# Kernel optimization log

Hardware: AMD Instinct MI355X
Metric: run time of the kernel (lower is better)

## Reference

```python
import jax, jax.numpy as jnp
import numpy as np

B, N, D = 256, 128, 128            # batch, tree nodes (incl. zero-pad node 0), input_feature_dim
MAX_PRED, MAX_COL, MAX_OP = 30, 200, 20
OTHER = D - 2 * MAX_PRED - 1 - 32  # 35
C_IN = D + 64 - 2 * MAX_PRED - 1   # 131 = tree-conv input channels


def setup_inputs() -> dict:
    key = jax.random.key(0)
    ks = jax.random.split(key, 14)
    others = jax.random.normal(ks[0], (B, N, OTHER), dtype=jnp.float32)
    cols = jax.random.randint(ks[1], (B, N, MAX_PRED), 0, MAX_COL).astype(jnp.float32)
    ops = jax.random.randint(ks[2], (B, N, MAX_PRED), 0, MAX_OP).astype(jnp.float32)
    length = jax.random.randint(ks[3], (B, N, 1), 0, MAX_PRED + 1).astype(jnp.float32)
    param = jax.random.normal(ks[4], (B, N, 32), dtype=jnp.float32)
    feature = jnp.concatenate([others, cols, ops, length, param], axis=-1).transpose(0, 2, 1)  # (B, D, N)
    indexes = jax.random.randint(ks[5], (B, 3 * (N - 1), 1), 0, N, dtype=jnp.int32).astype(jnp.int64)

    def conv_w(k, o, i):
        return jax.random.normal(k, (o, i, 3), dtype=jnp.float32) * (1.0 / np.sqrt(3 * i))

    def lin_w(k, o, i):
        return jax.random.normal(k, (o, i), dtype=jnp.float32) * (1.0 / np.sqrt(i))

    return dict(
        feature=feature, indexes=indexes,
        col_embed=jax.random.normal(ks[6], (MAX_COL, 32), dtype=jnp.float32),
        op_embed=jax.random.normal(ks[7], (MAX_OP, 32), dtype=jnp.float32),
        w1=conv_w(ks[8], 256, C_IN), b1=jnp.zeros((256,), jnp.float32),
        w2=conv_w(ks[9], 128, 256), b2=jnp.zeros((128,), jnp.float32),
        w3=conv_w(ks[10], 64, 128), b3=jnp.zeros((64,), jnp.float32),
        fw1=lin_w(ks[11], 32, 64), fb1=jnp.zeros((32,), jnp.float32),
        fw2=lin_w(ks[12], 1, 32), fb2=jnp.zeros((1,), jnp.float32),
    )


def tree_conv(x, idx, w, b):
    # x: (B, C, N); idx: (B, 3M, 1) with M = N-1; w: (O, C, 3)
    Bb, C, _ = x.shape
    g = jnp.take_along_axis(x, idx[:, :, 0][:, None, :], axis=2)        # (B, C, 3M) gather (self,left,right)
    g = g.reshape(Bb, C, -1, 3)                                          # (B, C, M, 3)
    out = jnp.einsum('bcmk,ock->bom', g, w) + b[None, :, None]           # stride-3 kernel-3 conv
    zero = jnp.zeros((Bb, w.shape[0], 1), out.dtype)                     # re-prepend zero-pad node
    return jnp.concatenate([zero, out], axis=2)                          # (B, O, N)


def tree_norm(x):
    # per-sample layernorm over (channel, node) dims, unbiased std (torch.std default)
    mean = jnp.mean(x, axis=(1, 2), keepdims=True)
    std = jnp.std(x, axis=(1, 2), ddof=1, keepdims=True)
    return (x - mean) / (std + 1e-5)


def reference(feature, indexes, col_embed, op_embed, w1, b1, w2, b2, w3, b3, fw1, fb1, fw2, fb2):
    Bb, d, n = feature.shape
    f = feature.transpose(0, 2, 1).reshape(Bb * n, d)
    others = f[:, :OTHER]
    cols = jax.lax.stop_gradient(f[:, OTHER:OTHER + MAX_PRED]).astype(jnp.int32)
    ops = jax.lax.stop_gradient(f[:, OTHER + MAX_PRED:OTHER + 2 * MAX_PRED]).astype(jnp.int32)
    length = f[:, OTHER + 2 * MAX_PRED:OTHER + 2 * MAX_PRED + 1]          # (BN, 1)
    param = f[:, -32:]
    emb = jnp.concatenate([col_embed[cols], op_embed[ops]], axis=-1)      # (BN, P, 64)
    mask = jnp.arange(MAX_PRED)[None, :] < length                         # (BN, P)
    total = jnp.sum(emb * mask[..., None], axis=1)                        # (BN, 64) masked sum
    collate = jnp.concatenate([others, total, param], axis=-1).reshape(Bb, n, -1).transpose(0, 2, 1)  # (B, C_IN, N)

    x = jax.nn.leaky_relu(tree_norm(tree_conv(collate, indexes, w1, b1)), 0.01)
    x = jax.nn.leaky_relu(tree_norm(tree_conv(x, indexes, w2, b2)), 0.01)
    x = tree_norm(tree_conv(x, indexes, w3, b3))                          # (B, 64, N)
    pooled = jnp.max(x, axis=2)                                           # DynamicPooling -> (B, 64)
    h = jax.nn.relu(pooled @ fw1.T + fb1)
    return h @ fw2.T + fb2                                                # (B, 1)
```

## Files before the change

kernel.cpp:

```cpp
#include <hip/hip_runtime.h>
#include <hip/hip_bf16.h>
#include <math.h>

#define B_    256
#define N_    128
#define MAXP  30
#define OTHER_ 35
#define CIN1  131
#define NIDX  381

#define KPAD1 160
#define KPAD2 256
#define KPAD3 128
#define S_IDX (B_ * NIDX)
#define S_P1  (15 * 4 * 4 * 512)
#define S_P2  (24 * 4 * 2 * 512)
#define S_P3  (12 * 4 * 1 * 512)
#define PREP_TOTAL (S_IDX + S_P1 + S_P2 + S_P3)
#define PREP_BLOCKS ((PREP_TOTAL + 511) / 512)
#define EMBED_BLOCKS (B_ * 4)

typedef short short8 __attribute__((ext_vector_type(8)));
typedef float f32x4 __attribute__((ext_vector_type(4)));

__device__ inline void split1(float v, short& h, short& l) {
  unsigned u = __float_as_uint(v);
  unsigned hb = (u + 0x7fffu + ((u >> 16) & 1u)) >> 16;
  float fh = __uint_as_float(hb << 16);
  float r = v - fh;
  unsigned u2 = __float_as_uint(r);
  unsigned lb = (u2 + 0x7fffu + ((u2 >> 16) & 1u)) >> 16;
  h = (short)hb;
  l = (short)lb;
}

__device__ inline void split2(float v, short& h, short& l) {
  __hip_bfloat16 hb = __float2bfloat16(v);
  float fh = __bfloat162float(hb);
  __hip_bfloat16 lb = __float2bfloat16(v - fh);
  __builtin_memcpy(&h, &hb, 2);
  __builtin_memcpy(&l, &lb, 2);
}

template <int KREAL, int KPAD, int SUB, int NWO>
__device__ inline void packw(int l, const float* __restrict__ w,
                             short* __restrict__ oh, short* __restrict__ ol) {
  const int e = l & 7;
  const int lane = (l >> 3) & 63;
  const int x = l >> 9;
  const int su = x % SUB;
  const int y = x / SUB;
  const int g = y % NWO;
  const int gks = y / NWO;
  const int oc = (g * SUB + su) * 16 + (lane & 15);
  const int ctot = gks * 32 + ((lane >> 4) & 3) * 8 + e;
  const int kk = ctot / KPAD;
  const int ch = ctot - kk * KPAD;
  const float v = (ch < KREAL) ? w[(oc * KREAL + ch) * 3 + kk] : 0.f;
  short h, lo;
  split1(v, h, lo);
  oh[l] = h;
  ol[l] = lo;
}

__global__ __launch_bounds__(512) void prep_embed_kernel(
    const float* __restrict__ feature,
    const float* __restrict__ col_embed,
    const float* __restrict__ op_embed,
    short* __restrict__ collateH, short* __restrict__ collateL,
    const void* __restrict__ rawIdx, int* __restrict__ idx32,
    const float* __restrict__ w1, short* __restrict__ w1h, short* __restrict__ w1l,
    const float* __restrict__ w2, short* __restrict__ w2h, short* __restrict__ w2l,
    const float* __restrict__ w3, short* __restrict__ w3h, short* __restrict__ w3l) {
  const int bx = blockIdx.x;
  const int tid = threadIdx.x;

  if (bx >= EMBED_BLOCKS) {
    const int gid = (bx - EMBED_BLOCKS) * 512 + tid;
    if (gid < S_IDX) {
      const int* r32 = (const int*)rawIdx;
      const int lane = tid & 63;
      const int lo = r32[2 * lane];
      const int hi = r32[2 * lane + 1];
      const bool ok = (hi == 0 && lo >= 0 && lo < N_);
      const bool is64 = __all(ok);
      idx32[gid] = is64 ? (int)((const long long*)rawIdx)[gid] : ((const int*)rawIdx)[gid];
    } else if (gid < S_IDX + S_P1) {
      packw<131, KPAD1, 4, 4>(gid - S_IDX, w1, w1h, w1l);
    } else if (gid < S_IDX + S_P1 + S_P2) {
      packw<256, KPAD2, 2, 4>(gid - (S_IDX + S_P1), w2, w2h, w2l);
    } else if (gid < PREP_TOTAL) {
      packw<128, KPAD3, 1, 4>(gid - (S_IDX + S_P1 + S_P2), w3, w3h, w3l);
    }
    return;
  }

  __shared__ float feat[128 * 33];
  __shared__ float ce[200 * 32];
  __shared__ float oe[20 * 32];
  const int b = bx >> 2;
  const int n0 = (bx & 3) * 32;
  const float* fb = feature + (size_t)b * 16384;

  {
    const float4* s = (const float4*)col_embed;
    float4* d = (float4*)ce;
#pragma unroll
    for (int it = 0; it < 4; ++it) {
      const int t = it * 512 + tid;
      if (t < 1600) d[t] = s[t];
    }
    if (tid < 160) ((float4*)oe)[tid] = ((const float4*)op_embed)[tid];
  }
  {
    const int d = tid >> 2;
    const int c8 = (tid & 3) * 8;
    const float4 v0 = *reinterpret_cast<const float4*>(&fb[d * 128 + n0 + c8]);
    const float4 v1 = *reinterpret_cast<const float4*>(&fb[d * 128 + n0 + c8 + 4]);
    float* p = &feat[d * 33 + c8];
    p[0] = v0.x; p[1] = v0.y; p[2] = v0.z; p[3] = v0.w;
    p[4] = v1.x; p[5] = v1.y; p[6] = v1.z; p[7] = v1.w;
  }
  __syncthreads();

  const int wv = tid >> 6;
  const int lane = tid & 63;
  const int cl = lane & 31;

#pragma unroll
  for (int ni = 0; ni < 4; ++ni) {
    const int nl = wv * 4 + ni;
    const int n = n0 + nl;
    int civ = 0, oiv = 0;
    if (lane < MAXP) civ = (int)feat[(OTHER_ + lane) * 33 + nl];
    if (lane >= 32 && lane < 32 + MAXP) oiv = (int)feat[(OTHER_ + MAXP + (lane - 32)) * 33 + nl];
    const int L = (int)feat[95 * 33 + nl];

    float acc = 0.f;
    for (int i = 0; i < L; ++i) {
      const int cv = __shfl(civ, i);
      const int ov = __shfl(oiv, 32 + i);
      acc += (lane < 32) ? ce[cv * 32 + cl] : oe[ov * 32 + cl];
    }

    short* outH = collateH + ((size_t)b * 128 + n) * KPAD1;
    short* outL = collateL + ((size_t)b * 128 + n) * KPAD1;
    short h, l;
    split2(acc, h, l);
    outH[35 + lane] = h; outL[35 + lane] = l;
    if (lane < 35) {
      split2(feat[lane * 33 + nl], h, l);
      outH[lane] = h; outL[lane] = l;
    }
    if (lane < 32) {
      split2(feat[(96 + lane) * 33 + nl], h, l);
      outH[99 + lane] = h; outL[99 + lane] = l;
    }
    if (lane < 29) { outH[131 + lane] = 0; outL[131 + lane] = 0; }
  }
}

__global__ __launch_bounds__(1024, 1) void fused_kernel(
    const short* __restrict__ XH, const short* __restrict__ XL,
    const int* __restrict__ idx,
    const short* __restrict__ w1h, const short* __restrict__ w1l,
    const short* __restrict__ w2h, const short* __restrict__ w2l,
    const short* __restrict__ w3h, const short* __restrict__ w3l,
    const float* __restrict__ b1, const float* __restrict__ b2,
    const float* __restrict__ b3,
    const float* __restrict__ fw1, const float* __restrict__ fb1,
    const float* __restrict__ fw2, const float* __restrict__ fb2,
    float* __restrict__ out) {
  constexpr int CINP = 264;

  __shared__ short sH[128 * CINP];
  __shared__ short sL[128 * CINP];
  __shared__ int nb_s[NIDX];
  __shared__ double red[32];
  __shared__ float bc[2];
  __shared__ float poolw[16][16];

  const int b = blockIdx.x;
  const int tid = threadIdx.x;
  const int lane = tid & 63;
  const int w = tid >> 6;
  const int wj = w >> 2;
  const int wo = w & 3;
  const int col = lane & 15;
  const int grp = (lane >> 4) & 3;
  const int jbase = wj * 32;

  const short8* __restrict__ wp1h = (const short8*)w1h;
  const short8* __restrict__ wp1l = (const short8*)w1l;
  const short8* __restrict__ wp2h = (const short8*)w2h;
  const short8* __restrict__ wp2l = (const short8*)w2l;
  const short8* __restrict__ wp3h = (const short8*)w3h;
  const short8* __restrict__ wp3l = (const short8*)w3l;

  auto blockStats = [&](double ss, double sq, double cnt) {
#pragma unroll
    for (int o = 32; o > 0; o >>= 1) {
      ss += __shfl_down(ss, o, 64);
      sq += __shfl_down(sq, o, 64);
    }
    if (lane == 0) { red[w * 2] = ss; red[w * 2 + 1] = sq; }
    __syncthreads();
    if (tid == 0) {
      double S = 0.0, Q = 0.0;
#pragma unroll
      for (int i = 0; i < 16; ++i) { S += red[i * 2]; Q += red[i * 2 + 1]; }
      const double m = S / cnt;
      double var = (Q - S * S / cnt) / (cnt - 1.0);
      if (var < 0.0) var = 0.0;
      bc[0] = (float)m;
      bc[1] = (float)(1.0 / (sqrt(var) + 1e-5));
    }
    __syncthreads();
  };

  {
    const short* __restrict__ XHb = XH + (size_t)b * (128 * KPAD1);
    const short* __restrict__ XLb = XL + (size_t)b * (128 * KPAD1);
#pragma unroll
    for (int it = 0; it < 3; ++it) {
      const int t = it * 1024 + tid;
      if (t < 128 * 20) {
        const int n = t / 20;
        const int c0 = (t - n * 20) * 8;
        *reinterpret_cast<short8*>(&sH[n * CINP + c0]) =
            *reinterpret_cast<const short8*>(&XHb[n * KPAD1 + c0]);
        *reinterpret_cast<short8*>(&sL[n * CINP + c0]) =
            *reinterpret_cast<const short8*>(&XLb[n * KPAD1 + c0]);
      }
    }
  }
  if (tid < NIDX) nb_s[tid] = idx[b * NIDX + tid];
  __syncthreads();

  int nbr[2][3];
#pragma unroll
  for (int jt = 0; jt < 2; ++jt) {
    const int jA = jbase + jt * 16 + col;
#pragma unroll
    for (int kk = 0; kk < 3; ++kk)
      nbr[jt][kk] = (jA > 0) ? nb_s[(jA - 1) * 3 + kk] : 0;
  }

  f32x4 a1[2][4];
#pragma unroll
  for (int jt = 0; jt < 2; ++jt)
#pragma unroll
    for (int su = 0; su < 4; ++su) {
      a1[jt][su][0] = 0.f; a1[jt][su][1] = 0.f;
      a1[jt][su][2] = 0.f; a1[jt][su][3] = 0.f;
    }

#pragma unroll
  for (int kk = 0; kk < 3; ++kk) {
#pragma unroll
    for (int ks = 0; ks < 5; ++ks) {
      const int gks = kk * 5 + ks;
      short8 ah[2], al[2];
#pragma unroll
      for (int jt = 0; jt < 2; ++jt) {
        const int ei = nbr[jt][kk] * CINP + ks * 32 + grp * 8;
        ah[jt] = *reinterpret_cast<const short8*>(&sH[ei]);
        al[jt] = *reinterpret_cast<const short8*>(&sL[ei]);
      }
      short8 bh[4], bl[4];
#pragma unroll
      for (int su = 0; su < 4; ++su) {
        const int wi = ((gks * 4 + wo) * 4 + su) * 64 + lane;
        bh[su] = wp1h[wi];
        bl[su] = wp1l[wi];
      }
#pragma unroll
      for (int jt = 0; jt < 2; ++jt)
#pragma unroll
        for (int su = 0; su < 4; ++su) {
          a1[jt][su] = __builtin_amdgcn_mfma_f32_16x16x32_bf16(ah[jt], bh[su], a1[jt][su], 0, 0, 0);
          a1[jt][su] = __builtin_amdgcn_mfma_f32_16x16x32_bf16(al[jt], bh[su], a1[jt][su], 0, 0, 0);
          a1[jt][su] = __builtin_amdgcn_mfma_f32_16x16x32_bf16(ah[jt], bl[su], a1[jt][su], 0, 0, 0);
        }
    }
  }

  {
    double ss = 0.0, sq = 0.0;
#pragma unroll
    for (int su = 0; su < 4; ++su) {
      const float bv = b1[(wo * 4 + su) * 16 + col];
#pragma unroll
      for (int jt = 0; jt < 2; ++jt)
#pragma unroll
        for (int r = 0; r < 4; ++r) {
          const int j = jbase + jt * 16 + grp * 4 + r;
          const float val = (j > 0) ? a1[jt][su][r] + bv : 0.f;
          a1[jt][su][r] = val;
          ss += (double)val;
          sq += (double)val * (double)val;
        }
    }
    blockStats(ss, sq, 256.0 * 128.0);
  }
  const float mean1 = bc[0], inv1 = bc[1];

#pragma unroll
  for (int su = 0; su < 4; ++su) {
    const int c = (wo * 4 + su) * 16 + col;
#pragma unroll
    for (int jt = 0; jt < 2; ++jt)
#pragma unroll
      for (int r = 0; r < 4; ++r) {
        const int j = jbase + jt * 16 + grp * 4 + r;
        float v = (a1[jt][su][r] - mean1) * inv1;
        v = fmaxf(v, 0.01f * v);
        short h, l;
        split2(v, h, l);
        sH[j * CINP + c] = h;
        sL[j * CINP + c] = l;
      }
  }
  __syncthreads();

  f32x4 a2[2][2];
#pragma unroll
  for (int jt = 0; jt < 2; ++jt)
#pragma unroll
    for (int su = 0; su < 2; ++su) {
      a2[jt][su][0] = 0.f; a2[jt][su][1] = 0.f;
      a2[jt][su][2] = 0.f; a2[jt][su][3] = 0.f;
    }

#pragma unroll
  for (int kk = 0; kk < 3; ++kk) {
#pragma unroll
    for (int ks = 0; ks < 8; ++ks) {
      const int gks = kk * 8 + ks;
      short8 ah[2], al[2];
#pragma unroll
      for (int jt = 0; jt < 2; ++jt) {
        const int ei = nbr[jt][kk] * CINP + ks * 32 + grp * 8;
        ah[jt] = *reinterpret_cast<const short8*>(&sH[ei]);
        al[jt] = *reinterpret_cast<const short8*>(&sL[ei]);
      }
      short8 bh[2], bl[2];
#pragma unroll
      for (int su = 0; su < 2; ++su) {
        const int wi = ((gks * 4 + wo) * 2 + su) * 64 + lane;
        bh[su] = wp2h[wi];
        bl[su] = wp2l[wi];
      }
#pragma unroll
      for (int jt = 0; jt < 2; ++jt)
#pragma unroll
        for (int su = 0; su < 2; ++su) {
          a2[jt][su] = __builtin_amdgcn_mfma_f32_16x16x32_bf16(ah[jt], bh[su], a2[jt][su], 0, 0, 0);
          a2[jt][su] = __builtin_amdgcn_mfma_f32_16x16x32_bf16(al[jt], bh[su], a2[jt][su], 0, 0, 0);
          a2[jt][su] = __builtin_amdgcn_mfma_f32_16x16x32_bf16(ah[jt], bl[su], a2[jt][su], 0, 0, 0);
        }
    }
  }

  {
    double ss = 0.0, sq = 0.0;
#pragma unroll
    for (int su = 0; su < 2; ++su) {
      const float bv = b2[(wo * 2 + su) * 16 + col];
#pragma unroll
      for (int jt = 0; jt < 2; ++jt)
#pragma unroll
        for (int r = 0; r < 4; ++r) {
          const int j = jbase + jt * 16 + grp * 4 + r;
          const float val = (j > 0) ? a2[jt][su][r] + bv : 0.f;
          a2[jt][su][r] = val;
          ss += (double)val;
          sq += (double)val * (double)val;
        }
    }
    blockStats(ss, sq, 128.0 * 128.0);
  }
  const float mean2 = bc[0], inv2 = bc[1];

#pragma unroll
  for (int su = 0; su < 2; ++su) {
    const int c = (wo * 2 + su) * 16 + col;
#pragma unroll
    for (int jt = 0; jt < 2; ++jt)
#pragma unroll
      for (int r = 0; r < 4; ++r) {
        const int j = jbase + jt * 16 + grp * 4 + r;
        float v = (a2[jt][su][r] - mean2) * inv2;
        v = fmaxf(v, 0.01f * v);
        short h, l;
        split2(v, h, l);
        sH[j * CINP + c] = h;
        sL[j * CINP + c] = l;
      }
  }
  __syncthreads();

  f32x4 a3[2];
#pragma unroll
  for (int jt = 0; jt < 2; ++jt) {
    a3[jt][0] = 0.f; a3[jt][1] = 0.f; a3[jt][2] = 0.f; a3[jt][3] = 0.f;
  }

#pragma unroll
  for (int kk = 0; kk < 3; ++kk) {
#pragma unroll
    for (int ks = 0; ks < 4; ++ks) {
      const int gks = kk * 4 + ks;
      short8 ah[2], al[2];
#pragma unroll
      for (int jt = 0; jt < 2; ++jt) {
        const int ei = nbr[jt][kk] * CINP + ks * 32 + grp * 8;
        ah[jt] = *reinterpret_cast<const short8*>(&sH[ei]);
        al[jt] = *reinterpret_cast<const short8*>(&sL[ei]);
      }
      short8 bh, bl;
      {
        const int wi = (gks * 4 + wo) * 64 + lane;
        bh = wp3h[wi];
        bl = wp3l[wi];
      }
#pragma unroll
      for (int jt = 0; jt < 2; ++jt) {
        a3[jt] = __builtin_amdgcn_mfma_f32_16x16x32_bf16(ah[jt], bh, a3[jt], 0, 0, 0);
        a3[jt] = __builtin_amdgcn_mfma_f32_16x16x32_bf16(al[jt], bh, a3[jt], 0, 0, 0);
        a3[jt] = __builtin_amdgcn_mfma_f32_16x16x32_bf16(ah[jt], bl, a3[jt], 0, 0, 0);
      }
    }
  }

  {
    double ss = 0.0, sq = 0.0;
    const float bv = b3[wo * 16 + col];
#pragma unroll
    for (int jt = 0; jt < 2; ++jt)
#pragma unroll
      for (int r = 0; r < 4; ++r) {
        const int j = jbase + jt * 16 + grp * 4 + r;
        const float val = (j > 0) ? a3[jt][r] + bv : 0.f;
        a3[jt][r] = val;
        ss += (double)val;
        sq += (double)val * (double)val;
      }
    blockStats(ss, sq, 64.0 * 128.0);
  }
  const float mean3 = bc[0], inv3 = bc[1];

  {
    float pm = -3.4e38f;
#pragma unroll
    for (int jt = 0; jt < 2; ++jt)
#pragma unroll
      for (int r = 0; r < 4; ++r)
        pm = fmaxf(pm, (a3[jt][r] - mean3) * inv3);
    pm = fmaxf(pm, __shfl_xor(pm, 16, 64));
    pm = fmaxf(pm, __shfl_xor(pm, 32, 64));
    if (lane < 16) poolw[w][col] = pm;
  }
  __syncthreads();

  if (w == 0) {
    float hval = 0.f;
    if (lane < 32) {
      float a = fb1[lane];
#pragma unroll 8
      for (int c = 0; c < 64; ++c) {
        const int oq = c >> 4, oc16 = c & 15;
        float p = poolw[oq][oc16];
#pragma unroll
        for (int jw = 1; jw < 4; ++jw) p = fmaxf(p, poolw[jw * 4 + oq][oc16]);
        a = fmaf(p, fw1[lane * 64 + c], a);
      }
      hval = fmaxf(a, 0.f) * fw2[lane];
    }
#pragma unroll
    for (int o = 32; o > 0; o >>= 1) hval += __shfl_down(hval, o, 64);
    if (lane == 0) out[b] = hval + fb2[0];
  }
}

extern "C" void kernel_launch(void* const* d_in, const int* in_sizes, int n_in,
                              void* d_out, int out_size, void* d_ws, size_t ws_size,
                              hipStream_t stream) {
  const float* feature   = (const float*)d_in[0];
  const void*  indexes   = d_in[1];
  const float* col_embed = (const float*)d_in[2];
  const float* op_embed  = (const float*)d_in[3];
  const float* w1  = (const float*)d_in[4];
  const float* b1  = (const float*)d_in[5];
  const float* w2  = (const float*)d_in[6];
  const float* b2  = (const float*)d_in[7];
  const float* w3  = (const float*)d_in[8];
  const float* b3  = (const float*)d_in[9];
  const float* fw1 = (const float*)d_in[10];
  const float* fb1 = (const float*)d_in[11];
  const float* fw2 = (const float*)d_in[12];
  const float* fb2 = (const float*)d_in[13];
  float* out = (float*)d_out;

  char* ws = (char*)d_ws;
  size_t off = 0;
  auto carve = [&](size_t bytes) -> char* {
    off = (off + 255) & ~(size_t)255;
    char* p = ws + off;
    off += bytes;
    return p;
  };
  int*   idx32    = (int*)carve((size_t)S_IDX * sizeof(int));
  short* w1h      = (short*)carve((size_t)S_P1 * sizeof(short));
  short* w1l      = (short*)carve((size_t)S_P1 * sizeof(short));
  short* w2h      = (short*)carve((size_t)S_P2 * sizeof(short));
  short* w2l      = (short*)carve((size_t)S_P2 * sizeof(short));
  short* w3h      = (short*)carve((size_t)S_P3 * sizeof(short));
  short* w3l      = (short*)carve((size_t)S_P3 * sizeof(short));
  short* collateH = (short*)carve((size_t)B_ * 128 * KPAD1 * sizeof(short));
  short* collateL = (short*)carve((size_t)B_ * 128 * KPAD1 * sizeof(short));
  (void)ws_size; (void)in_sizes; (void)n_in; (void)out_size;

  hipLaunchKernelGGL(prep_embed_kernel, dim3(EMBED_BLOCKS + PREP_BLOCKS), dim3(512), 0, stream,
                     feature, col_embed, op_embed, collateH, collateL,
                     indexes, idx32, w1, w1h, w1l, w2, w2h, w2l, w3, w3h, w3l);
  hipLaunchKernelGGL(fused_kernel, dim3(B_), dim3(1024), 0, stream,
                     collateH, collateL, idx32,
                     w1h, w1l, w2h, w2l, w3h, w3l,
                     b1, b2, b3, fw1, fb1, fw2, fb2, out);
}
```

Measured before the change: 84.23 us.

## Fuse embedding collate into the fused tree-conv kernel via shared memory

The embedding lookup, masked sum and bf16 hi/lo split that built the collate tensor move from the prep kernel into the main per-batch kernel. The results are written straight into the shared-memory tiles, reusing the same LDS region for the raw feature and embedding tables first. This removes the global write and re-read of the split collate buffers and shrinks the prep kernel. In exchange, the main kernel runs extra serial work and barriers before its first conv, and only 256 blocks now do the embedding work instead of 1024.

Measured after the change: 79.41 us (median of 2 runs). 1.06x faster.

```diff
diff --git a/kernel.cpp b/kernel.cpp
--- a/kernel.cpp
+++ b/kernel.cpp
@@ -18,7 +18,6 @@
 #define S_P3  (12 * 4 * 1 * 512)
 #define PREP_TOTAL (S_IDX + S_P1 + S_P2 + S_P3)
 #define PREP_BLOCKS ((PREP_TOTAL + 511) / 512)
-#define EMBED_BLOCKS (B_ * 4)
 
 typedef short short8 __attribute__((ext_vector_type(8)));
 typedef float f32x4 __attribute__((ext_vector_type(4)));
@@ -63,105 +62,33 @@
   ol[l] = lo;
 }
 
-__global__ __launch_bounds__(512) void prep_embed_kernel(
-    const float* __restrict__ feature,
-    const float* __restrict__ col_embed,
-    const float* __restrict__ op_embed,
-    short* __restrict__ collateH, short* __restrict__ collateL,
+__global__ __launch_bounds__(512) void prep_kernel(
     const void* __restrict__ rawIdx, int* __restrict__ idx32,
     const float* __restrict__ w1, short* __restrict__ w1h, short* __restrict__ w1l,
     const float* __restrict__ w2, short* __restrict__ w2h, short* __restrict__ w2l,
     const float* __restrict__ w3, short* __restrict__ w3h, short* __restrict__ w3l) {
-  const int bx = blockIdx.x;
-  const int tid = threadIdx.x;
-
-  if (bx >= EMBED_BLOCKS) {
-    const int gid = (bx - EMBED_BLOCKS) * 512 + tid;
-    if (gid < S_IDX) {
-      const int* r32 = (const int*)rawIdx;
-      const int lane = tid & 63;
-      const int lo = r32[2 * lane];
-      const int hi = r32[2 * lane + 1];
-      const bool ok = (hi == 0 && lo >= 0 && lo < N_);
-      const bool is64 = __all(ok);
-      idx32[gid] = is64 ? (int)((const long long*)rawIdx)[gid] : ((const int*)rawIdx)[gid];
-    } else if (gid < S_IDX + S_P1) {
-      packw<131, KPAD1, 4, 4>(gid - S_IDX, w1, w1h, w1l);
-    } else if (gid < S_IDX + S_P1 + S_P2) {
-      packw<256, KPAD2, 2, 4>(gid - (S_IDX + S_P1), w2, w2h, w2l);
-    } else if (gid < PREP_TOTAL) {
-      packw<128, KPAD3, 1, 4>(gid - (S_IDX + S_P1 + S_P2), w3, w3h, w3l);
-    }
-    return;
-  }
-
-  __shared__ float feat[128 * 33];
-  __shared__ float ce[200 * 32];
-  __shared__ float oe[20 * 32];
-  const int b = bx >> 2;
-  const int n0 = (bx & 3) * 32;
-  const float* fb = feature + (size_t)b * 16384;
-
-  {
-    const float4* s = (const float4*)col_embed;
-    float4* d = (float4*)ce;
-#pragma unroll
-    for (int it = 0; it < 4; ++it) {
-      const int t = it * 512 + tid;
-      if (t < 1600) d[t] = s[t];
-    }
-    if (tid < 160) ((float4*)oe)[tid] = ((const float4*)op_embed)[tid];
-  }
-  {
-    const int d = tid >> 2;
-    const int c8 = (tid & 3) * 8;
-    const float4 v0 = *reinterpret_cast<const float4*>(&fb[d * 128 + n0 + c8]);
-    const float4 v1 = *reinterpret_cast<const float4*>(&fb[d * 128 + n0 + c8 + 4]);
-    float* p = &feat[d * 33 + c8];
-    p[0] = v0.x; p[1] = v0.y; p[2] = v0.z; p[3] = v0.w;
-    p[4] = v1.x; p[5] = v1.y; p[6] = v1.z; p[7] = v1.w;
-  }
-  __syncthreads();
-
-  const int wv = tid >> 6;
-  const int lane = tid & 63;
-  const int cl = lane & 31;
-
-#pragma unroll
-  for (int ni = 0; ni < 4; ++ni) {
-    const int nl = wv * 4 + ni;
-    const int n = n0 + nl;
-    int civ = 0, oiv = 0;
-    if (lane < MAXP) civ = (int)feat[(OTHER_ + lane) * 33 + nl];
-    if (lane >= 32 && lane < 32 + MAXP) oiv = (int)feat[(OTHER_ + MAXP + (lane - 32)) * 33 + nl];
-    const int L = (int)feat[95 * 33 + nl];
-
-    float acc = 0.f;
-    for (int i = 0; i < L; ++i) {
-      const int cv = __shfl(civ, i);
-      const int ov = __shfl(oiv, 32 + i);
-      acc += (lane < 32) ? ce[cv * 32 + cl] : oe[ov * 32 + cl];
-    }
-
-    short* outH = collateH + ((size_t)b * 128 + n) * KPAD1;
-    short* outL = collateL + ((size_t)b * 128 + n) * KPAD1;
-    short h, l;
-    split2(acc, h, l);
-    outH[35 + lane] = h; outL[35 + lane] = l;
-    if (lane < 35) {
-      split2(feat[lane * 33 + nl], h, l);
-      outH[lane] = h; outL[lane] = l;
-    }
-    if (lane < 32) {
-      split2(feat[(96 + lane) * 33 + nl], h, l);
-      outH[99 + lane] = h; outL[99 + lane] = l;
-    }
-    if (lane < 29) { outH[131 + lane] = 0; outL[131 + lane] = 0; }
+  const int gid = blockIdx.x * 512 + threadIdx.x;
+  if (gid < S_IDX) {
+    const int* r32 = (const int*)rawIdx;
+    const int lane = threadIdx.x & 63;
+    const int lo = r32[2 * lane];
+    const int hi = r32[2 * lane + 1];
+    const bool ok = (hi == 0 && lo >= 0 && lo < N_);
+    const bool is64 = __all(ok);
+    idx32[gid] = is64 ? (int)((const long long*)rawIdx)[gid] : ((const int*)rawIdx)[gid];
+  } else if (gid < S_IDX + S_P1) {
+    packw<131, KPAD1, 4, 4>(gid - S_IDX, w1, w1h, w1l);
+  } else if (gid < S_IDX + S_P1 + S_P2) {
+    packw<256, KPAD2, 2, 4>(gid - (S_IDX + S_P1), w2, w2h, w2l);
+  } else if (gid < PREP_TOTAL) {
+    packw<128, KPAD3, 1, 4>(gid - (S_IDX + S_P1 + S_P2), w3, w3h, w3l);
   }
 }
 
 __global__ __launch_bounds__(1024, 1) void fused_kernel(
-    const short* __restrict__ XH, const short* __restrict__ XL,
+    const float* __restrict__ feature,
+    const float* __restrict__ col_embed,
+    const float* __restrict__ op_embed,
     const int* __restrict__ idx,
     const short* __restrict__ w1h, const short* __restrict__ w1l,
     const short* __restrict__ w2h, const short* __restrict__ w2l,
@@ -173,12 +100,17 @@
     float* __restrict__ out) {
   constexpr int CINP = 264;
 
-  __shared__ short sH[128 * CINP];
-  __shared__ short sL[128 * CINP];
+  __shared__ short smem[128 * CINP * 2];
   __shared__ int nb_s[NIDX];
   __shared__ double red[32];
   __shared__ float bc[2];
   __shared__ float poolw[16][16];
+
+  short* sH = smem;
+  short* sL = smem + 128 * CINP;
+  float* feat = (float*)smem;
+  float* ceL  = ((float*)smem) + 128 * 133;
+  float* oeL  = ceL + 200 * 32;
 
   const int b = blockIdx.x;
   const int tid = threadIdx.x;
@@ -189,6 +121,7 @@
   const int col = lane & 15;
   const int grp = (lane >> 4) & 3;
   const int jbase = wj * 32;
+  const int cl = lane & 31;
 
   const short8* __restrict__ wp1h = (const short8*)w1h;
   const short8* __restrict__ wp1l = (const short8*)w1l;
@@ -219,24 +152,46 @@
   };
 
   {
-    const short* __restrict__ XHb = XH + (size_t)b * (128 * KPAD1);
-    const short* __restrict__ XLb = XL + (size_t)b * (128 * KPAD1);
-#pragma unroll
-    for (int it = 0; it < 3; ++it) {
+    const float* fb = feature + (size_t)b * 16384;
+#pragma unroll
+    for (int it = 0; it < 4; ++it) {
       const int t = it * 1024 + tid;
-      if (t < 128 * 20) {
-        const int n = t / 20;
-        const int c0 = (t - n * 20) * 8;
-        *reinterpret_cast<short8*>(&sH[n * CINP + c0]) =
-            *reinterpret_cast<const short8*>(&XHb[n * KPAD1 + c0]);
-        *reinterpret_cast<short8*>(&sL[n * CINP + c0]) =
-            *reinterpret_cast<const short8*>(&XLb[n * KPAD1 + c0]);
-      }
-    }
-  }
-  if (tid < NIDX) nb_s[tid] = idx[b * NIDX + tid];
+      const int d = t >> 5;
+      const int c4 = (t & 31) * 4;
+      const float4 v = *reinterpret_cast<const float4*>(&fb[d * 128 + c4]);
+      float* p = &feat[d * 133 + c4];
+      p[0] = v.x; p[1] = v.y; p[2] = v.z; p[3] = v.w;
+    }
+    const float4* s = (const float4*)col_embed;
+    float4* d4 = (float4*)ceL;
+#pragma unroll
+    for (int it = 0; it < 2; ++it) {
+      const int t = it * 1024 + tid;
+      if (t < 1600) d4[t] = s[t];
+    }
+    if (tid < 160) ((float4*)oeL)[tid] = ((const float4*)op_embed)[tid];
+    if (tid < NIDX) nb_s[tid] = idx[b * NIDX + tid];
+  }
   __syncthreads();
 
+  float emb[8], oth[8], par[8];
+#pragma unroll
+  for (int ni = 0; ni < 8; ++ni) {
+    const int n = w * 8 + ni;
+    int civ = 0, oiv = 0;
+    if (lane < MAXP) civ = (int)feat[(OTHER_ + lane) * 133 + n];
+    if (lane >= 32 && lane < 32 + MAXP) oiv = (int)feat[(OTHER_ + MAXP + (lane - 32)) * 133 + n];
+    const int L = (int)feat[95 * 133 + n];
+    float acc = 0.f;
+    for (int i = 0; i < L; ++i) {
+      const int cv = __shfl(civ, i);
+      const int ov = __shfl(oiv, 32 + i);
+      acc += (lane < 32) ? ceL[cv * 32 + cl] : oeL[ov * 32 + cl];
+    }
+    emb[ni] = acc;
+    oth[ni] = (lane < 35) ? feat[lane * 133 + n] : 0.f;
+    par[ni] = (lane < 32) ? feat[(96 + lane) * 133 + n] : 0.f;
+  }
   int nbr[2][3];
 #pragma unroll
   for (int jt = 0; jt < 2; ++jt) {
@@ -245,6 +200,26 @@
     for (int kk = 0; kk < 3; ++kk)
       nbr[jt][kk] = (jA > 0) ? nb_s[(jA - 1) * 3 + kk] : 0;
   }
+  __syncthreads();
+
+#pragma unroll
+  for (int ni = 0; ni < 8; ++ni) {
+    const int n = w * 8 + ni;
+    const int base = n * CINP;
+    short h, l;
+    split2(emb[ni], h, l);
+    sH[base + 35 + lane] = h; sL[base + 35 + lane] = l;
+    if (lane < 35) {
+      split2(oth[ni], h, l);
+      sH[base + lane] = h; sL[base + lane] = l;
+    }
+    if (lane < 32) {
+      split2(par[ni], h, l);
+      sH[base + 99 + lane] = h; sL[base + 99 + lane] = l;
+    }
+    if (lane < 29) { sH[base + 131 + lane] = 0; sL[base + 131 + lane] = 0; }
+  }
+  __syncthreads();
 
   f32x4 a1[2][4];
 #pragma unroll
@@ -510,22 +485,19 @@
     off += bytes;
     return p;
   };
-  int*   idx32    = (int*)carve((size_t)S_IDX * sizeof(int));
-  short* w1h      = (short*)carve((size_t)S_P1 * sizeof(short));
-  short* w1l      = (short*)carve((size_t)S_P1 * sizeof(short));
-  short* w2h      = (short*)carve((size_t)S_P2 * sizeof(short));
-  short* w2l      = (short*)carve((size_t)S_P2 * sizeof(short));
-  short* w3h      = (short*)carve((size_t)S_P3 * sizeof(short));
-  short* w3l      = (short*)carve((size_t)S_P3 * sizeof(short));
-  short* collateH = (short*)carve((size_t)B_ * 128 * KPAD1 * sizeof(short));
-  short* collateL = (short*)carve((size_t)B_ * 128 * KPAD1 * sizeof(short));
+  int*   idx32 = (int*)carve((size_t)S_IDX * sizeof(int));
+  short* w1h   = (short*)carve((size_t)S_P1 * sizeof(short));
+  short* w1l   = (short*)carve((size_t)S_P1 * sizeof(short));
+  short* w2h   = (short*)carve((size_t)S_P2 * sizeof(short));
+  short* w2l   = (short*)carve((size_t)S_P2 * sizeof(short));
+  short* w3h   = (short*)carve((size_t)S_P3 * sizeof(short));
+  short* w3l   = (short*)carve((size_t)S_P3 * sizeof(short));
   (void)ws_size; (void)in_sizes; (void)n_in; (void)out_size;
 
-  hipLaunchKernelGGL(prep_embed_kernel, dim3(EMBED_BLOCKS + PREP_BLOCKS), dim3(512), 0, stream,
-                     feature, col_embed, op_embed, collateH, collateL,
+  hipLaunchKernelGGL(prep_kernel, dim3(PREP_BLOCKS), dim3(512), 0, stream,
                      indexes, idx32, w1, w1h, w1l, w2, w2h, w2l, w3, w3h, w3l);
   hipLaunchKernelGGL(fused_kernel, dim3(B_), dim3(1024), 0, stream,
-                     collateH, collateL, idx32,
+                     feature, col_embed, op_embed, idx32,
                      w1h, w1l, w2h, w2l, w3h, w3l,
                      b1, b2, b3, fw1, fb1, fw2, fb2, out);
 }
```
